# Kernel tuning notes

Measured on AMD Instinct MI355X. Metric: run time of the kernel, lower is better.

Reference implementation:

```python
import jax, jax.numpy as jnp
import numpy as np

EMBED_DIM = 64
D_STATE = 16
D_CONV = 4
EXPAND = 2
DT_RANK = 8
D_INNER = EXPAND * EMBED_DIM  # 128
B_, T_, H_, W_ = 4, 16, 16, 16


def _causal_dwconv(x, w, b):
    # x: (B, D, L), w: (D, 1, K) depthwise causal conv (left pad K-1), matches
    # torch conv1d(padding=K-1)[..., :L]
    K = w.shape[-1]
    y = jax.lax.conv_general_dilated(
        x, w, window_strides=(1,), padding=[(K - 1, 0)],
        feature_group_count=x.shape[1], dimension_numbers=('NCH', 'OIH', 'NCH'))
    return y + b[None, :, None]


def _selective_scan(u, delta, A, Bm, Cm, D):
    # u, delta: (B, d, L); A: (d, n); Bm, Cm: (B, n, L); D: (d,)
    dA = jnp.exp(jnp.einsum('bdl,dn->lbdn', delta, A))      # (L,B,d,n)
    dBu = jnp.einsum('bdl,bnl,bdl->lbdn', delta, Bm, u)     # (L,B,d,n)
    h0 = jnp.zeros(dA.shape[1:], dA.dtype)

    def step(h, xs):
        dA_t, dBu_t = xs
        h = dA_t * h + dBu_t
        return h, h

    _, hs = jax.lax.scan(step, h0, (dA, dBu))               # (L,B,d,n)
    y = jnp.einsum('lbdn,bnl->bdl', hs, Cm)
    return y + u * D[None, :, None]


def _mamba_branch(x, z, conv_w, conv_b, xproj_w, dtproj_w, dtproj_b, A_log, D):
    # x, z: (B, d_inner, L)
    x = jax.nn.silu(_causal_dwconv(x, conv_w, conv_b))
    x_dbl = jnp.einsum('bdl,ed->bel', x, xproj_w)           # e = dt_rank + 2*n
    dt = x_dbl[:, :DT_RANK]
    Bm = x_dbl[:, DT_RANK:DT_RANK + D_STATE]
    Cm = x_dbl[:, DT_RANK + D_STATE:]
    delta = jax.nn.softplus(jnp.einsum('brl,dr->bdl', dt, dtproj_w) + dtproj_b[None, :, None])
    A = -jnp.exp(A_log)
    y = _selective_scan(x, delta, A, Bm, Cm, D)
    return y * jax.nn.silu(z)


def _conv3d(x, w, b, pad):
    y = jax.lax.conv_general_dilated(
        x, w, window_strides=(1, 1, 1), padding=[(pad, pad)] * 3,
        dimension_numbers=('NCDHW', 'OIDHW', 'NCDHW'))
    return y + b[None, :, None, None, None]


def setup_inputs() -> dict:
    key = jax.random.key(0)
    ks = jax.random.split(key, 24)
    s = 0.02
    d, n, r, K, C = D_INNER, D_STATE, DT_RANK, D_CONV, EMBED_DIM
    inp = {
        'x': jax.random.normal(ks[0], (B_, C, T_, H_, W_), jnp.float32),
        'in_proj_w': jax.random.normal(ks[1], (2 * d, C), jnp.float32) * s,
        'conv_w': jax.random.normal(ks[2], (d, 1, K), jnp.float32) * s,
        'conv_b': jnp.zeros((d,), jnp.float32),
        'xproj_w': jax.random.normal(ks[3], (r + 2 * n, d), jnp.float32) * s,
        'dtproj_w': jax.random.normal(ks[4], (d, r), jnp.float32) * s,
        'dtproj_b': jax.random.normal(ks[5], (d,), jnp.float32) * s,
        'A_log': jnp.tile(jnp.log(jnp.arange(1, n + 1, dtype=jnp.float32))[None, :], (d, 1)),
        'D': jnp.ones((d,), jnp.float32),
        'conv_w_b': jax.random.normal(ks[6], (d, 1, K), jnp.float32) * s,
        'conv_b_b': jnp.zeros((d,), jnp.float32),
        'xproj_w_b': jax.random.normal(ks[7], (r + 2 * n, d), jnp.float32) * s,
        'dtproj_w_b': jax.random.normal(ks[8], (d, r), jnp.float32) * s,
        'dtproj_b_b': jax.random.normal(ks[9], (d,), jnp.float32) * s,
        'A_b_log': jnp.tile(jnp.log(jnp.arange(1, n + 1, dtype=jnp.float32))[None, :], (d, 1)),
        'D_b': jnp.ones((d,), jnp.float32),
        'out_proj_w': jax.random.normal(ks[10], (C, d), jnp.float32) * s,
        'proj_w': jax.random.normal(ks[11], (C, C, 3, 3, 3), jnp.float32) * s,
        'proj_b': jnp.zeros((C,), jnp.float32),
        'norm_w': jax.random.normal(ks[12], (C, C, 1, 1, 1), jnp.float32) * s,
        'norm_b': jnp.zeros((C,), jnp.float32),
    }
    return inp


def reference(x, in_proj_w, conv_w, conv_b, xproj_w, dtproj_w, dtproj_b, A_log, D,
              conv_w_b, conv_b_b, xproj_w_b, dtproj_w_b, dtproj_b_b, A_b_log, D_b,
              out_proj_w, proj_w, proj_b, norm_w, norm_b):
    residual = x
    B, C, T, H, W = x.shape
    # SpectralPriority scan: b c t h w -> b c (h w t)
    seq = x.transpose(0, 1, 3, 4, 2).reshape(B, C, H * W * T)
    # bimamba v2
    xz = jnp.einsum('bcl,ec->bel', seq, in_proj_w)          # (B, 2*d_inner, L)
    x_f, z_f = xz[:, :D_INNER], xz[:, D_INNER:]
    y_f = _mamba_branch(x_f, z_f, conv_w, conv_b, xproj_w, dtproj_w, dtproj_b, A_log, D)
    xz_r = jnp.flip(xz, -1)
    x_b, z_b = xz_r[:, :D_INNER], xz_r[:, D_INNER:]
    y_b = _mamba_branch(x_b, z_b, conv_w_b, conv_b_b, xproj_w_b, dtproj_w_b, dtproj_b_b, A_b_log, D_b)
    out = y_f + jnp.flip(y_b, -1)                           # (B, d_inner, L)
    out = jnp.einsum('bdl,cd->blc', out, out_proj_w)        # (B, L, C)
    x_recon = out.reshape(B, C, T, H, W)
    x3 = _conv3d(x_recon, proj_w, proj_b, pad=1)
    return _conv3d(x3 + residual, norm_w, norm_b, pad=0)
```

## Files before the change

kernel.cpp:

```cpp
#include <hip/hip_runtime.h>


#define NL 4096

typedef unsigned short u16;
typedef unsigned int u32;
typedef __attribute__((ext_vector_type(8))) short bf16x8;
typedef __attribute__((ext_vector_type(4))) float f32x4;

__device__ __forceinline__ float siluf_(float x) {
  return x * __builtin_amdgcn_rcpf(1.f + __expf(-x));
}
__device__ __forceinline__ float softplusf_(float x) {
  return (x > 20.f) ? x : __logf(1.f + __expf(x));
}
__device__ __forceinline__ u16 f2bf(float f) {
  u32 u = __float_as_uint(f);
  u += 0x7fffu + ((u >> 16) & 1u);
  return (u16)(u >> 16);
}

#define DPPADD(ctl, x) \
  { int q_ = __builtin_amdgcn_mov_dpp(__float_as_int(x), ctl, 0xf, 0xf, false); \
    x += __int_as_float(q_); }

#define OXZ  0u
#define OUCF 1048576u
#define OUCB 1572864u
#define ODLF 2424832u
#define ODLB 2949120u
#define OYF  3473408u
#define OYB  3997696u
#define OO   4521984u
#define OO2  5046272u
#define PER_B 5570560u

#define NCH 64
#define CL  64
#define WB1 110592u

__global__ __launch_bounds__(256) void kxz(
    const float* __restrict__ x, const float* __restrict__ wip,
    float* __restrict__ ws, int b0) {
  int bi = blockIdx.y, gb = b0 + bi;
  float* s = ws + (size_t)bi * PER_B;
  int bid = blockIdx.x;
  int h = bid >> 4, w = bid & 15;
  int tid = threadIdx.x;
  __shared__ float xs[64][16];
  for (int i = tid; i < 1024; i += 256) {
    int c = i >> 4, t = i & 15;
    xs[c][t] = x[(size_t)(gb * 64 + c) * NL + t * 256 + h * 16 + w];
  }
  __syncthreads();
  int e = tid;
  float acc[16];
#pragma unroll
  for (int t = 0; t < 16; ++t) acc[t] = 0.f;
  for (int c = 0; c < 64; ++c) {
    float wv = wip[e * 64 + c];
#pragma unroll
    for (int t = 0; t < 16; ++t) acc[t] = fmaf(wv, xs[c][t], acc[t]);
  }
  float4* dst = (float4*)(s + OXZ + (size_t)e * NL + h * 256 + w * 16);
#pragma unroll
  for (int q = 0; q < 4; ++q)
    dst[q] = make_float4(acc[q * 4], acc[q * 4 + 1], acc[q * 4 + 2], acc[q * 4 + 3]);
}

__global__ __launch_bounds__(256) void k2prep(
    const float* __restrict__ cwf, const float* __restrict__ cbf,
    const float* __restrict__ xpf, const float* __restrict__ dtwf,
    const float* __restrict__ dtbf,
    const float* __restrict__ cwb, const float* __restrict__ cbb,
    const float* __restrict__ xpb, const float* __restrict__ dtwb,
    const float* __restrict__ dtbb,
    float* __restrict__ ws) {
  int bi = blockIdx.y;
  float* s = ws + (size_t)bi * PER_B;
  int bx = blockIdx.x;
  int lt = bx >> 1, dir = bx & 1;
  int l0 = lt * 32;
  int lout0 = dir ? (127 - lt) * 32 : l0;
  int tid = threadIdx.x;

  __shared__ float pool[128 * 40];
  __shared__ u16 uct[32][136];
  float (*X)[40] = (float(*)[40])pool;

  for (int i = tid; i < 128 * 38; i += 256) {
    int d = i / 38, j = i - d * 38;
    int l = l0 - 3 + j;
    X[d][j] = (l >= 0 && l < NL) ? s[OXZ + (size_t)d * NL + l] : 0.f;
  }
  __syncthreads();

  const float* cw = dir ? cwb : cwf;
  const float* cb = dir ? cbb : cbf;
  float* ucg = s + (dir ? OUCB : OUCF);
  for (int i = tid; i < 128 * 32; i += 256) {
    int d = i >> 5, li = i & 31;
    float a = cb[d];
    if (dir == 0) {
#pragma unroll
      for (int k = 0; k < 4; ++k) a = fmaf(cw[d * 4 + k], X[d][li + k], a);
    } else {
#pragma unroll
      for (int k = 0; k < 4; ++k) a = fmaf(cw[d * 4 + k], X[d][37 - li - k], a);
    }
    a = siluf_(a);
    uct[li][d] = f2bf(a);
    ucg[(size_t)d * NL + lout0 + li] = a;
  }
  __syncthreads();

  float* xds = pool;
  {
    int wid = tid >> 6, lane = tid & 63;
    int n16 = lane & 15, kg = lane >> 4;
    const float* xp = dir ? xpb : xpf;
#pragma unroll
    for (int rep = 0; rep < 2; ++rep) {
      int id = wid + rep * 4;
      if (id < 6) {
        int et = id >> 1, lt2 = id & 1;
        f32x4 acc = {};
#pragma unroll
        for (int ks = 0; ks < 4; ++ks) {
          bf16x8 bfrag = *(const bf16x8*)&uct[lt2 * 16 + n16][ks * 32 + kg * 8];
          int e = et * 16 + n16;
          int ec = (e < 40) ? e : 39;
          const float* pa = xp + ec * 128 + ks * 32 + kg * 8;
          float4 a0 = *(const float4*)pa;
          float4 a1 = *(const float4*)(pa + 4);
          bf16x8 af;
          af[0] = (short)f2bf(a0.x); af[1] = (short)f2bf(a0.y);
          af[2] = (short)f2bf(a0.z); af[3] = (short)f2bf(a0.w);
          af[4] = (short)f2bf(a1.x); af[5] = (short)f2bf(a1.y);
          af[6] = (short)f2bf(a1.z); af[7] = (short)f2bf(a1.w);
          acc = __builtin_amdgcn_mfma_f32_16x16x32_bf16(af, bfrag, acc, 0, 0, 0);
        }
#pragma unroll
        for (int rg = 0; rg < 4; ++rg) {
          int e = et * 16 + kg * 4 + rg;
          if (e < 40) xds[e * 33 + lt2 * 16 + n16] = acc[rg];
        }
      }
    }
  }
  __syncthreads();

  const float* dtw = dir ? dtwb : dtwf;
  const float* dtb = dir ? dtbb : dtbf;
  float* dlg = s + (dir ? ODLB : ODLF);
  for (int i = tid; i < 128 * 32; i += 256) {
    int d = i >> 5, li = i & 31;
    float pre = dtb[d];
#pragma unroll
    for (int r = 0; r < 8; ++r)
      pre = fmaf(dtw[d * 8 + r], xds[r * 33 + li], pre);
    dlg[(size_t)d * NL + lout0 + li] = softplusf_(pre);
  }
  u16* bctp = (u16*)(s + OO2);
  for (int i = tid; i < 32 * 32; i += 256) {
    int li = i >> 5, k = i & 31;
    bctp[((size_t)dir * 4096 + lout0 + li) * 32 + k] = f2bf(xds[(8 + k) * 33 + li]);
  }
}

__global__ __launch_bounds__(256) void kscanA(
    const float* __restrict__ Alf, const float* __restrict__ Alb,
    float* __restrict__ ws) {
  int bi = blockIdx.y;
  float* s = ws + (size_t)bi * PER_B;
  int xid = blockIdx.x;
  int chunk = xid >> 4, dir = (xid >> 3) & 1, d8 = xid & 7;
  int tid = threadIdx.x;
  int wv = tid >> 6, lane = tid & 63;
  int n = lane & 15, g = lane >> 4;
  int d = d8 * 16 + wv * 4 + g;
  int l0 = chunk * CL;
  __shared__ float bl[CL * 16];
  {
    const u16* bctp = (const u16*)(s + OO2) + ((size_t)dir * 4096 + l0) * 32;
    for (int i = tid; i < CL * 16; i += 256) {
      int l = i >> 4, k = i & 15;
      bl[i] = __uint_as_float(((u32)bctp[l * 32 + k]) << 16);
    }
  }
  __syncthreads();
  const float* ucp = s + (dir ? OUCB : OUCF) + (size_t)d * NL + l0;
  const float* dlp = s + (dir ? ODLB : ODLF) + (size_t)d * NL + l0;
  const float* blB = bl + n;
  float A = -__expf((dir ? Alb : Alf)[d * 16 + n]);
  float P = 1.f, S = 0.f;
#pragma unroll
  for (int i0 = 0; i0 < CL; i0 += 8) {
    float4 dq0 = *(const float4*)(dlp + i0);
    float4 dq1 = *(const float4*)(dlp + i0 + 4);
    float4 uq0 = *(const float4*)(ucp + i0);
    float4 uq1 = *(const float4*)(ucp + i0 + 4);
    float dv[8] = {dq0.x, dq0.y, dq0.z, dq0.w, dq1.x, dq1.y, dq1.z, dq1.w};
    float uv[8] = {uq0.x, uq0.y, uq0.z, uq0.w, uq1.x, uq1.y, uq1.z, uq1.w};
#pragma unroll
    for (int j = 0; j < 8; ++j) {
      float dA = __expf(dv[j] * A);
      S = fmaf(dA, S, dv[j] * blB[(i0 + j) * 16] * uv[j]);
      P *= dA;
    }
  }
  size_t cidx = ((size_t)(chunk * 2 + dir) * 128 + d) * 16 + n;
  s[OO + cidx] = P;
  s[OO + 262144u + cidx] = S;
}

__global__ __launch_bounds__(256) void kscanC(
    const float* __restrict__ Alf, const float* __restrict__ Df,
    const float* __restrict__ Alb, const float* __restrict__ Db,
    float* __restrict__ ws) {
  int bi = blockIdx.y;
  float* s = ws + (size_t)bi * PER_B;
  int xid = blockIdx.x;
  int chunk = xid >> 4, dir = (xid >> 3) & 1, d8 = xid & 7;
  int tid = threadIdx.x;
  int wv = tid >> 6, lane = tid & 63;
  int n = lane & 15, g = lane >> 4;
  int d = d8 * 16 + wv * 4 + g;
  int l0 = chunk * CL;
  __shared__ float bl[CL * 32];
  __shared__ float ps[16][65];
  {
    const u16* bctp = (const u16*)(s + OO2) + ((size_t)dir * 4096 + l0) * 32;
    for (int i = tid; i < CL * 32; i += 256)
      bl[i] = __uint_as_float(((u32)bctp[i]) << 16);
  }
  __syncthreads();
  const float* ucp = s + (dir ? OUCB : OUCF) + (size_t)d * NL + l0;
  const float* dlp = s + (dir ? ODLB : ODLF) + (size_t)d * NL + l0;
  const float* blB = bl + n;
  float* ybase = s + (dir ? OYB : OYF);
  float A = -__expf((dir ? Alb : Alf)[d * 16 + n]);
  float Dv = (dir ? Db : Df)[d];
  float h = 0.f;
  {
    size_t stepi = (size_t)d * 16 + n;
#pragma unroll 4
    for (int c = 0; c < chunk; ++c) {
      size_t idx = ((size_t)(c * 2 + dir) * 128) * 16 + stepi;
      float pv = s[OO + idx], sv = s[OO + 262144u + idx];
      h = fmaf(pv, h, sv);
    }
  }
  int prow = wv * 4 + g;
#pragma unroll
  for (int i0 = 0; i0 < CL; i0 += 8) {
    float4 dq0 = *(const float4*)(dlp + i0);
    float4 dq1 = *(const float4*)(dlp + i0 + 4);
    float4 uq0 = *(const float4*)(ucp + i0);
    float4 uq1 = *(const float4*)(ucp + i0 + 4);
    float dv[8] = {dq0.x, dq0.y, dq0.z, dq0.w, dq1.x, dq1.y, dq1.z, dq1.w};
    float uv[8] = {uq0.x, uq0.y, uq0.z, uq0.w, uq1.x, uq1.y, uq1.z, uq1.w};
    float hv[8];
#pragma unroll
    for (int j = 0; j < 8; ++j) {
      float dA = __expf(dv[j] * A);
      h = fmaf(dA, h, dv[j] * blB[(i0 + j) * 32] * uv[j]);
      hv[j] = h * blB[(i0 + j) * 32 + 16];
    }
#pragma unroll
    for (int j = 0; j < 8; ++j) DPPADD(0x121, hv[j])
#pragma unroll
    for (int j = 0; j < 8; ++j) DPPADD(0x122, hv[j])
#pragma unroll
    for (int j = 0; j < 8; ++j) DPPADD(0x124, hv[j])
#pragma unroll
    for (int j = 0; j < 8; ++j) DPPADD(0x128, hv[j])
    if (n == 0) {
#pragma unroll
      for (int j = 0; j < 8; ++j)
        ps[prow][i0 + j] = fmaf(uv[j], Dv, hv[j]);
    }
  }
  __syncthreads();
  for (int i = tid; i < 16 * CL; i += 256) {
    int row = i >> 6, col = i & 63;
    ybase[(size_t)(d8 * 16 + row) * NL + l0 + col] = ps[row][col];
  }
}

__global__ __launch_bounds__(256) void koutg(
    const float* __restrict__ wout, float* __restrict__ ws) {
  int bi = blockIdx.y;
  float* s = ws + (size_t)bi * PER_B;
  int lt = blockIdx.x;
  int l0 = lt * 32;
  int tid = threadIdx.x;
  __shared__ u16 otb[32][136];
  for (int i = tid; i < 128 * 32; i += 256) {
    int d = i >> 5, li = i & 31;
    int l = l0 + li;
    float z = s[OXZ + (size_t)(128 + d) * NL + l];
    float v = s[OYF + (size_t)d * NL + l] + s[OYB + (size_t)d * NL + (NL - 1 - l)];
    otb[li][d] = f2bf(v * siluf_(z));
  }
  __syncthreads();
  int wid = tid >> 6, lane = tid & 63;
  int n16 = lane & 15, kg = lane >> 4;
  f32x4 acc[2] = {};
  const float* wr = wout + (size_t)(wid * 16 + n16) * 128 + kg * 8;
#pragma unroll
  for (int ks = 0; ks < 4; ++ks) {
    const float* pa = wr + ks * 32;
    float4 a0 = *(const float4*)pa;
    float4 a1 = *(const float4*)(pa + 4);
    bf16x8 af;
    af[0] = (short)f2bf(a0.x); af[1] = (short)f2bf(a0.y);
    af[2] = (short)f2bf(a0.z); af[3] = (short)f2bf(a0.w);
    af[4] = (short)f2bf(a1.x); af[5] = (short)f2bf(a1.y);
    af[6] = (short)f2bf(a1.z); af[7] = (short)f2bf(a1.w);
    bf16x8 b0 = *(const bf16x8*)&otb[n16][ks * 32 + kg * 8];
    bf16x8 b1 = *(const bf16x8*)&otb[16 + n16][ks * 32 + kg * 8];
    acc[0] = __builtin_amdgcn_mfma_f32_16x16x32_bf16(af, b0, acc[0], 0, 0, 0);
    acc[1] = __builtin_amdgcn_mfma_f32_16x16x32_bf16(af, b1, acc[1], 0, 0, 0);
  }
#pragma unroll
  for (int l2 = 0; l2 < 2; ++l2) {
    float4 st = make_float4(acc[l2][0], acc[l2][1], acc[l2][2], acc[l2][3]);
    *(float4*)&s[OO2 + (size_t)(l0 + l2 * 16 + n16) * 64 + wid * 16 + kg * 4] = st;
  }
}

__global__ __launch_bounds__(256) void kprepw(
    const float* __restrict__ pw, float* __restrict__ wdst) {
  int off = blockIdx.x;
  u16* wb = (u16*)wdst;
  int tid = threadIdx.x;
  for (int i = tid; i < 4096; i += 256) {
    int co = i >> 6, ci = i & 63;
    u16 v = f2bf(pw[(size_t)(co * 64 + ci) * 27 + off]);
#pragma unroll
    for (int xc = 0; xc < 8; ++xc)
      wb[(size_t)xc * WB1 + off * 4096 + i] = v;
  }
}

__global__ __launch_bounds__(256, 2) void kconv3(
    const float* __restrict__ pb, const float* __restrict__ nw,
    const float* __restrict__ nb, const float* __restrict__ xin,
    float* __restrict__ out, const u16* __restrict__ wb,
    float* __restrict__ ws, int b0) {
  int bi = blockIdx.y, gb = b0 + bi;
  float* s = ws + (size_t)bi * PER_B;
  int bx = blockIdx.x;
  int t = bx >> 3, hq = bx & 7;
  int h0 = hq * 2;
  int tid = threadIdx.x;
  const float* xr = s + OO2;

  __shared__ u16 Xs[3 * 4 * 18 * 72];
  float* cx = (float*)Xs;
  {
    u32* xz32 = (u32*)Xs;
    for (int i = tid; i < 3 * 4 * 18 * 72 / 2; i += 256) xz32[i] = 0u;
  }
  __syncthreads();
  {
    int ci = tid >> 2, wq = tid & 3;
#pragma unroll
    for (int rowc = 0; rowc < 12; ++rowc) {
      int tt = rowc >> 2, hh = rowc & 3;
      int ts = t + tt - 1, hs = h0 + hh - 1;
      if (ts < 0 || ts > 15 || hs < 0 || hs > 15) continue;
      float4 v = *(const float4*)(xr + (size_t)ci * NL + ts * 256 + hs * 16 + wq * 4);
      int rb = (tt * 4 + hh) * 18 + 1 + wq * 4;
      Xs[(rb + 0) * 72 + ci] = f2bf(v.x);
      Xs[(rb + 1) * 72 + ci] = f2bf(v.y);
      Xs[(rb + 2) * 72 + ci] = f2bf(v.z);
      Xs[(rb + 3) * 72 + ci] = f2bf(v.w);
    }
  }
  __syncthreads();

  int wid = tid >> 6, lane = tid & 63;
  int cq = wid;
  int n16 = lane & 15, kg = lane >> 4;
  f32x4 acc[2] = {};

  const u16* wbA = wb + (size_t)(bx & 7) * WB1 +
                   (size_t)(cq * 16 + n16) * 64 + kg * 8;
#pragma unroll
  for (int kt = 0; kt < 3; ++kt)
#pragma unroll
    for (int kh = 0; kh < 3; ++kh) {
#pragma unroll
      for (int kw = 0; kw < 3; ++kw) {
        int off = (kt * 3 + kh) * 3 + kw;
        const u16* pa = wbA + off * 4096;
#pragma unroll
        for (int st = 0; st < 2; ++st) {
          int kb = st * 32;
          bf16x8 a0 = *(const bf16x8*)(pa + kb);
#pragma unroll
          for (int l2 = 0; l2 < 2; ++l2) {
            int r = (kt * 4 + l2 + kh) * 18 + n16 + kw;
            bf16x8 b0 = *(const bf16x8*)(&Xs[r * 72 + kb + kg * 8]);
            acc[l2] = __builtin_amdgcn_mfma_f32_16x16x32_bf16(a0, b0, acc[l2], 0, 0, 0);
          }
        }
      }
    }
  __syncthreads();

#pragma unroll
  for (int l2 = 0; l2 < 2; ++l2) {
    int lp = l2 * 16 + n16;
    int lg = t * 256 + (h0 + l2) * 16 + n16;
#pragma unroll
    for (int rg = 0; rg < 4; ++rg) {
      int co = cq * 16 + kg * 4 + rg;
      cx[co * 33 + lp] = acc[l2][rg] + pb[co] +
                         xin[(size_t)(gb * 64 + co) * NL + lg];
    }
  }
  __syncthreads();

  {
    int co2 = tid >> 2, pq = tid & 3;
    float mac[8];
#pragma unroll
    for (int j = 0; j < 8; ++j) mac[j] = 0.f;
    for (int ci = 0; ci < 64; ci += 4) {
      float4 w4 = *(const float4*)&nw[co2 * 64 + ci];
      float wv[4] = {w4.x, w4.y, w4.z, w4.w};
#pragma unroll
      for (int cc = 0; cc < 4; ++cc) {
        const float* row = &cx[(ci + cc) * 33 + pq * 8];
        float4 a = *(const float4*)&row[0];
        float4 b = *(const float4*)&row[4];
        mac[0] = fmaf(wv[cc], a.x, mac[0]);  mac[1] = fmaf(wv[cc], a.y, mac[1]);
        mac[2] = fmaf(wv[cc], a.z, mac[2]);  mac[3] = fmaf(wv[cc], a.w, mac[3]);
        mac[4] = fmaf(wv[cc], b.x, mac[4]);  mac[5] = fmaf(wv[cc], b.y, mac[5]);
        mac[6] = fmaf(wv[cc], b.z, mac[6]);  mac[7] = fmaf(wv[cc], b.w, mac[7]);
      }
    }
    float bias = nb[co2];
    float4* dst = (float4*)(out + (size_t)(gb * 64 + co2) * NL +
                            t * 256 + h0 * 16 + pq * 8);
    dst[0] = make_float4(mac[0] + bias, mac[1] + bias, mac[2] + bias, mac[3] + bias);
    dst[1] = make_float4(mac[4] + bias, mac[5] + bias, mac[6] + bias, mac[7] + bias);
  }
}

extern "C" void kernel_launch(void* const* d_in, const int* in_sizes, int n_in,
                              void* d_out, int out_size, void* d_ws, size_t ws_size,
                              hipStream_t stream) {
  const float* x    = (const float*)d_in[0];
  const float* wip  = (const float*)d_in[1];
  const float* cwf  = (const float*)d_in[2];
  const float* cbf  = (const float*)d_in[3];
  const float* xpf  = (const float*)d_in[4];
  const float* dtwf = (const float*)d_in[5];
  const float* dtbf = (const float*)d_in[6];
  const float* Alf  = (const float*)d_in[7];
  const float* Df   = (const float*)d_in[8];
  const float* cwb  = (const float*)d_in[9];
  const float* cbb  = (const float*)d_in[10];
  const float* xpb  = (const float*)d_in[11];
  const float* dtwb = (const float*)d_in[12];
  const float* dtbb = (const float*)d_in[13];
  const float* Alb  = (const float*)d_in[14];
  const float* Db   = (const float*)d_in[15];
  const float* wout = (const float*)d_in[16];
  const float* pw   = (const float*)d_in[17];
  const float* pb   = (const float*)d_in[18];
  const float* nw   = (const float*)d_in[19];
  const float* nb   = (const float*)d_in[20];

  const size_t PER_B_BYTES = (size_t)PER_B * 4;
  const size_t WB_BYTES = 8u * WB1 * 2u;
  int bcnt;
  if (ws_size >= 4 * PER_B_BYTES + WB_BYTES) bcnt = 4;
  else if (ws_size >= PER_B_BYTES + WB_BYTES) bcnt = 1;
  else return;
  int passes = 4 / bcnt;

  float* ws = (float*)d_ws;
  float* wsW = ws + (size_t)bcnt * PER_B;
  kprepw<<<dim3(27), 256, 0, stream>>>(pw, wsW);
  for (int p = 0; p < passes; ++p) {
    int b0 = p * bcnt;
    kxz   <<<dim3(256, bcnt), 256, 0, stream>>>(x, wip, ws, b0);
    k2prep<<<dim3(256, bcnt), 256, 0, stream>>>(cwf, cbf, xpf, dtwf, dtbf,
                                                cwb, cbb, xpb, dtwb, dtbb, ws);
    kscanA<<<dim3(1024, bcnt), 256, 0, stream>>>(Alf, Alb, ws);
    kscanC<<<dim3(1024, bcnt), 256, 0, stream>>>(Alf, Df, Alb, Db, ws);
    koutg <<<dim3(128, bcnt), 256, 0, stream>>>(wout, ws);
    kconv3<<<dim3(128, bcnt), 256, 0, stream>>>(pb, nw, nb, x, (float*)d_out,
                                                (const u16*)wsW, ws, b0);
  }
}
```

Measured before the change: 258.2 us.

## Replace DPP reduction in chunk scan with LDS-staged C dot products

The chunk-summary kernel now accumulates the sum of delta and computes the decay product once as exp(A*sum), instead of multiplying 64 exponentials together. In the chunk-apply kernel, the per-step DPP butterfly reduction over the 16 state lanes is removed. Hidden states are written to shared memory in half-chunks, and each thread then computes full output dot products with C using float4 LDS reads, which also coalesces the y stores. This trades cross-lane DPP ops and the masked n==0 writes for extra LDS traffic and two more block barriers per half-chunk.

```diff
diff --git a/kernel.cpp b/kernel.cpp
--- a/kernel.cpp
+++ b/kernel.cpp
@@ -19,10 +19,6 @@
   u += 0x7fffu + ((u >> 16) & 1u);
   return (u16)(u >> 16);
 }
-
-#define DPPADD(ctl, x) \
-  { int q_ = __builtin_amdgcn_mov_dpp(__float_as_int(x), ctl, 0xf, 0xf, false); \
-    x += __int_as_float(q_); }
 
 #define OXZ  0u
 #define OUCF 1048576u
@@ -193,7 +189,7 @@
   const float* dlp = s + (dir ? ODLB : ODLF) + (size_t)d * NL + l0;
   const float* blB = bl + n;
   float A = -__expf((dir ? Alb : Alf)[d * 16 + n]);
-  float P = 1.f, S = 0.f;
+  float sdv = 0.f, S = 0.f;
 #pragma unroll
   for (int i0 = 0; i0 < CL; i0 += 8) {
     float4 dq0 = *(const float4*)(dlp + i0);
@@ -206,11 +202,11 @@
     for (int j = 0; j < 8; ++j) {
       float dA = __expf(dv[j] * A);
       S = fmaf(dA, S, dv[j] * blB[(i0 + j) * 16] * uv[j]);
-      P *= dA;
+      sdv += dv[j];
     }
   }
   size_t cidx = ((size_t)(chunk * 2 + dir) * 128 + d) * 16 + n;
-  s[OO + cidx] = P;
+  s[OO + cidx] = __expf(A * sdv);
   s[OO + 262144u + cidx] = S;
 }
 
@@ -228,19 +224,12 @@
   int d = d8 * 16 + wv * 4 + g;
   int l0 = chunk * CL;
   __shared__ float bl[CL * 32];
-  __shared__ float ps[16][65];
+  __shared__ float Chw[4][32][68];
   {
     const u16* bctp = (const u16*)(s + OO2) + ((size_t)dir * 4096 + l0) * 32;
     for (int i = tid; i < CL * 32; i += 256)
       bl[i] = __uint_as_float(((u32)bctp[i]) << 16);
   }
-  __syncthreads();
-  const float* ucp = s + (dir ? OUCB : OUCF) + (size_t)d * NL + l0;
-  const float* dlp = s + (dir ? ODLB : ODLF) + (size_t)d * NL + l0;
-  const float* blB = bl + n;
-  float* ybase = s + (dir ? OYB : OYF);
-  float A = -__expf((dir ? Alb : Alf)[d * 16 + n]);
-  float Dv = (dir ? Db : Df)[d];
   float h = 0.f;
   {
     size_t stepi = (size_t)d * 16 + n;
@@ -251,40 +240,58 @@
       h = fmaf(pv, h, sv);
     }
   }
-  int prow = wv * 4 + g;
-#pragma unroll
-  for (int i0 = 0; i0 < CL; i0 += 8) {
-    float4 dq0 = *(const float4*)(dlp + i0);
-    float4 dq1 = *(const float4*)(dlp + i0 + 4);
-    float4 uq0 = *(const float4*)(ucp + i0);
-    float4 uq1 = *(const float4*)(ucp + i0 + 4);
-    float dv[8] = {dq0.x, dq0.y, dq0.z, dq0.w, dq1.x, dq1.y, dq1.z, dq1.w};
-    float uv[8] = {uq0.x, uq0.y, uq0.z, uq0.w, uq1.x, uq1.y, uq1.z, uq1.w};
-    float hv[8];
-#pragma unroll
-    for (int j = 0; j < 8; ++j) {
-      float dA = __expf(dv[j] * A);
-      h = fmaf(dA, h, dv[j] * blB[(i0 + j) * 32] * uv[j]);
-      hv[j] = h * blB[(i0 + j) * 32 + 16];
-    }
-#pragma unroll
-    for (int j = 0; j < 8; ++j) DPPADD(0x121, hv[j])
-#pragma unroll
-    for (int j = 0; j < 8; ++j) DPPADD(0x122, hv[j])
-#pragma unroll
-    for (int j = 0; j < 8; ++j) DPPADD(0x124, hv[j])
-#pragma unroll
-    for (int j = 0; j < 8; ++j) DPPADD(0x128, hv[j])
-    if (n == 0) {
-#pragma unroll
-      for (int j = 0; j < 8; ++j)
-        ps[prow][i0 + j] = fmaf(uv[j], Dv, hv[j]);
-    }
-  }
-  __syncthreads();
-  for (int i = tid; i < 16 * CL; i += 256) {
-    int row = i >> 6, col = i & 63;
-    ybase[(size_t)(d8 * 16 + row) * NL + l0 + col] = ps[row][col];
+  __syncthreads();
+  const float* ucp = s + (dir ? OUCB : OUCF) + (size_t)d * NL + l0;
+  const float* dlp = s + (dir ? ODLB : ODLF) + (size_t)d * NL + l0;
+  const float* ucb0 = s + (dir ? OUCB : OUCF) + l0;
+  const float* blB = bl + n;
+  float* ybase = s + (dir ? OYB : OYF);
+  const float* Dvp = dir ? Db : Df;
+  float A = -__expf((dir ? Alb : Alf)[d * 16 + n]);
+
+#pragma unroll
+  for (int H = 0; H < 2; ++H) {
+#pragma unroll
+    for (int i0b = 0; i0b < 32; i0b += 8) {
+      int i0 = H * 32 + i0b;
+      float4 dq0 = *(const float4*)(dlp + i0);
+      float4 dq1 = *(const float4*)(dlp + i0 + 4);
+      float4 uq0 = *(const float4*)(ucp + i0);
+      float4 uq1 = *(const float4*)(ucp + i0 + 4);
+      float dv[8] = {dq0.x, dq0.y, dq0.z, dq0.w, dq1.x, dq1.y, dq1.z, dq1.w};
+      float uv[8] = {uq0.x, uq0.y, uq0.z, uq0.w, uq1.x, uq1.y, uq1.z, uq1.w};
+      float hv[8];
+#pragma unroll
+      for (int j = 0; j < 8; ++j) {
+        float dA = __expf(dv[j] * A);
+        h = fmaf(dA, h, dv[j] * blB[(i0 + j) * 32] * uv[j]);
+        hv[j] = h;
+      }
+#pragma unroll
+      for (int j = 0; j < 8; ++j) Chw[wv][i0b + j][g * 16 + n] = hv[j];
+    }
+    __syncthreads();
+#pragma unroll
+    for (int rep = 0; rep < 2; ++rep) {
+      int o = tid + rep * 256;
+      int l_o = o & 31, g_o = (o >> 5) & 3, wv_o = o >> 7;
+      int lc = H * 32 + l_o;
+      const float* hrow = &Chw[wv_o][l_o][g_o * 16];
+      const float* crow = &bl[lc * 32 + 16];
+      float y = 0.f;
+#pragma unroll
+      for (int q = 0; q < 4; ++q) {
+        float4 h4 = *(const float4*)(hrow + q * 4);
+        float4 c4 = *(const float4*)(crow + q * 4);
+        y = fmaf(h4.x, c4.x, y); y = fmaf(h4.y, c4.y, y);
+        y = fmaf(h4.z, c4.z, y); y = fmaf(h4.w, c4.w, y);
+      }
+      int d_o = d8 * 16 + wv_o * 4 + g_o;
+      float u = ucb0[(size_t)d_o * NL + lc];
+      y = fmaf(u, Dvp[d_o], y);
+      ybase[(size_t)d_o * NL + l0 + lc] = y;
+    }
+    __syncthreads();
   }
 }
 
```

New measurement: 275.6 us. 6.7% more time.
